# Performance work log

Hardware: AMD Instinct MI355X
Metric: run time of the kernel (lower is better)

The kernel has to match this reference:

```python
import jax, jax.numpy as jnp
import numpy as np

B, C, H, W = 8, 128, 128, 128
PLANES, K, STRIDE, PAD = 128, 3, 1, 1
BN_EPS = 1e-5


def setup_inputs() -> dict:
    key = jax.random.key(0)
    k1, k2, k3, k4 = jax.random.split(key, 4)
    x = jax.random.normal(k1, (B, C, H, W), jnp.float32)
    # ConvOffset2D: Conv2d(C, 2C, 3, pad=1, bias=False), weights ~ N(0, 0.01)
    w_off = jax.random.normal(k2, (2 * C, C, 3, 3), jnp.float32) * 0.01
    w_conv = jax.random.normal(k3, (PLANES, C, K, K), jnp.float32) * 0.05
    b_conv = jax.random.normal(k4, (PLANES,), jnp.float32) * 0.01
    gamma = jnp.ones((PLANES,), jnp.float32)
    beta = jnp.zeros((PLANES,), jnp.float32)
    return {"x": x, "w_off": w_off, "w_conv": w_conv, "b_conv": b_conv,
            "gamma": gamma, "beta": beta}


def _conv2d(x, w, stride, pad):
    return jax.lax.conv_general_dilated(
        x, w, window_strides=(stride, stride),
        padding=[(pad, pad), (pad, pad)],
        dimension_numbers=("NCHW", "OIHW", "NCHW"))


def _deform_sample(x, offsets):
    """x: (B,C,H,W); offsets: (B,2C,H,W) -> bilinear offset-sampled (B,C,H,W).
    Faithful to ConvOffset2D: raw reshape (b,2c,h,w) -> (b*c, h*w, 2),
    coords = offsets + meshgrid(i,j), clamp, bilinear interp."""
    b, c, h, w = x.shape
    off = offsets.reshape(b * c, h * w, 2)              # quirky but faithful reshape
    grid = jnp.stack(jnp.meshgrid(jnp.arange(h, dtype=x.dtype),
                                  jnp.arange(w, dtype=x.dtype),
                                  indexing="ij"), axis=-1).reshape(1, h * w, 2)
    coords = off + grid                                  # (b*c, h*w, 2)
    yc = jnp.clip(coords[..., 0], 0.0, h - 1.0)
    xc = jnp.clip(coords[..., 1], 0.0, w - 1.0)
    y0, y1 = jnp.floor(yc), jnp.ceil(yc)
    x0, x1 = jnp.floor(xc), jnp.ceil(xc)
    img = x.reshape(b * c, h * w)

    def gather(yy, xx):
        idx = (yy * w + xx).astype(jnp.int32)
        return jnp.take_along_axis(img, idx, axis=1)

    v_lt = gather(y0, x0)
    v_rb = gather(y1, x1)
    v_lb = gather(y0, x1)
    v_rt = gather(y1, x0)
    dy = yc - y0
    dx = xc - x0
    v_t = v_lt + (v_rt - v_lt) * dy   # interp along height
    v_b = v_lb + (v_rb - v_lb) * dy
    out = v_t + (v_b - v_t) * dx      # interp along width
    return out.reshape(b, c, h, w)


def reference(x, w_off, w_conv, b_conv, gamma, beta):
    offsets = _conv2d(x, w_off, 1, 1)                    # (B, 2C, H, W)
    x_off = _deform_sample(x, offsets)                   # (B, C, H, W)
    y = _conv2d(x_off, w_conv, STRIDE, PAD) + b_conv[None, :, None, None]
    y = jax.nn.relu(y)
    # BatchNorm2d in training mode: batch statistics, biased variance
    mean = y.mean(axis=(0, 2, 3), keepdims=True)
    var = jnp.square(y - mean).mean(axis=(0, 2, 3), keepdims=True)
    y = (y - mean) * jax.lax.rsqrt(var + BN_EPS)
    return y * gamma[None, :, None, None] + beta[None, :, None, None]
```

## Files before the change

### kernel.cpp

```cpp
#include <hip/hip_runtime.h>

#define B_   8
#define C_   128
#define H_   128
#define W_   128
#define HW_  16384

typedef short v8s __attribute__((ext_vector_type(8)));
typedef float v4f __attribute__((ext_vector_type(4)));

#define ROWB 4160

__device__ __forceinline__ float bf2f(unsigned short u) {
  unsigned int v = ((unsigned int)u) << 16;
  float f; __builtin_memcpy(&f, &v, 4); return f;
}
__device__ __forceinline__ unsigned short f2us(float f) {
  unsigned int u; __builtin_memcpy(&u, &f, 4);
  u += 0x7fffu + ((u >> 16) & 1u);
  return (unsigned short)(u >> 16);
}

__global__ __launch_bounds__(256) void pack_w(const float* __restrict__ w,
                                              unsigned short* __restrict__ pack,
                                              uint4* __restrict__ zb, int G) {
  if (blockIdx.x == 0) zb[threadIdx.x] = (uint4){0u, 0u, 0u, 0u};
  int idx = blockIdx.x * 256 + threadIdx.x;
  if (idx >= 20480 * G) return;
  int j  = idx & 7;
  int l  = (idx >> 3) & 63;
  int g  = (idx >> 9) % G;
  int t2 = idx / (512 * G);
  int pp = t2 % 5;
  int cc = t2 / 5;
  int oc = g * 16 + (l & 15);
  int kk = ((l >> 4) << 3) + j;
  int ic = (cc << 4) + (kk & 15);
  int rs = pp * 2 + (kk >> 4);
  float v = (rs < 9) ? w[(oc * C_ + ic) * 9 + rs] : 0.f;
  pack[idx] = f2us(v);
}

__global__ __launch_bounds__(256) void transpose_x(const float* __restrict__ x,
                                                   unsigned short* __restrict__ xt) {
  __shared__ alignas(16) unsigned short t[32 * 132];
  const int j0 = blockIdx.x * 32, i = blockIdx.y, b = blockIdx.z;
  const int tid = threadIdx.x;
  for (int e = tid; e < 128 * 32; e += 256) {
    int c = e >> 5, jj = e & 31;
    float v = x[((b * C_ + c) * H_ + i) * W_ + j0 + jj];
    t[jj * 132 + c] = f2us(v);
  }
  __syncthreads();
  for (int f = tid; f < 1024; f += 256) {
    int cg = f >> 7, g = f & 127;
    int j = g >> 2, c4 = (g & 3) << 2;
    uint2 v = *(const uint2*)&t[j * 132 + cg * 16 + c4];
    *(uint2*)(xt + ((size_t)(b * 8 + cg) * HW_ + i * W_ + j0 + j) * 16 + c4) = v;
  }
}

template <int MODE, int G>
__global__ __launch_bounds__(256) void conv_gemm(const unsigned short* __restrict__ xt,
                                                 const unsigned short* __restrict__ pack,
                                                 const float* __restrict__ bias,
                                                 const char* __restrict__ zb,
                                                 unsigned short* __restrict__ outp,
                                                 float* __restrict__ ps) {
  __shared__ alignas(16) char rawb[3 * ROWB];
  __shared__ float bs1[128], bs2[128];

  const int nb = blockIdx.x;
  int b, i, mt;
  {
    int xcd = nb & 7, r = nb >> 3;
    if (MODE == 0) { b = r >> 5; mt = (r >> 4) & 1; i = xcd * 16 + (r & 15); }
    else           { b = r >> 4; mt = 0;            i = xcd * 16 + (r & 15); }
  }
  const int tid  = threadIdx.x;
  const int lane = tid & 63, wid = tid >> 6;
  const int q = lane >> 4, n = lane & 15;
  const int wm = wid & 1, wn = wid >> 1;

  if (MODE == 1 && tid < 128) { bs1[tid] = 0.f; bs2[tid] = 0.f; }
  if (tid < 12) {
    int r = tid >> 2, rem = tid & 3, side = rem >> 1, h = rem & 1;
    *(uint4*)(rawb + r * ROWB + (side ? 129 * 32 : 0) + h * 16) = (uint4){0u,0u,0u,0u};
  }

  int boff[5];
#pragma unroll
  for (int pp = 0; pp < 5; ++pp) {
    int rs = pp * 2 + (q >> 1);
    if (rs > 8) rs = 8;
    int r = (rs >= 6) ? 2 : ((rs >= 3) ? 1 : 0);
    int s = rs - r * 3;
    boff[pp] = r * ROWB + s * 32 + (q & 1) * 16;
  }
  const int pcol = (wn * 64 + n) * 32;

  v4f acc[4][4];
#pragma unroll
  for (int a = 0; a < 4; ++a)
#pragma unroll
    for (int c = 0; c < 4; ++c) acc[a][c] = (v4f){0.f, 0.f, 0.f, 0.f};

  const v8s* packv = (const v8s*)pack;
  const int gbase = mt * 8 + wm * 4;

  v8s Acur[4];
  {
    const v8s* ap = packv + (0 * G + gbase) * 64 + lane;
#pragma unroll
    for (int fm = 0; fm < 4; ++fm) Acur[fm] = ap[fm * 64];
  }

  for (int cc = 0; cc < 8; ++cc) {
    __syncthreads();
    const char* ccbase = (const char*)xt + (size_t)(b * 8 + cc) * (HW_ * 32);
#pragma unroll
    for (int t = 0; t < 3; ++t) {
      int c = wid * 3 + t, r = c >> 2, k = c & 3;
      int ii = i + r - 1;
      const char* src = ((unsigned)ii < 128u)
                          ? ccbase + ii * 4096 + k * 1024 + lane * 16
                          : zb + lane * 16;
      __builtin_amdgcn_global_load_lds(
          (const __attribute__((address_space(1))) unsigned int*)src,
          (__attribute__((address_space(3))) unsigned int*)(rawb + r * ROWB + 32 + k * 1024),
          16, 0, 0);
    }
    __syncthreads();

#pragma unroll
    for (int pp = 0; pp < 5; ++pp) {
      v8s Anxt[4];
      const bool havenext = (pp < 4) || (cc < 7);
      if (havenext) {
        int ncc = (pp < 4) ? cc : cc + 1;
        int npp = (pp < 4) ? pp + 1 : 0;
        const v8s* ap = packv + ((ncc * 5 + npp) * G + gbase) * 64 + lane;
#pragma unroll
        for (int fm = 0; fm < 4; ++fm) Anxt[fm] = ap[fm * 64];
      }
      v8s Bf[4];
#pragma unroll
      for (int fn = 0; fn < 4; ++fn)
        Bf[fn] = *(const v8s*)(rawb + boff[pp] + pcol + fn * 512);
#pragma unroll
      for (int fm = 0; fm < 4; ++fm) {
#pragma unroll
        for (int fn = 0; fn < 4; ++fn)
          acc[fm][fn] = __builtin_amdgcn_mfma_f32_16x16x32_bf16(Acur[fm], Bf[fn],
                                                                acc[fm][fn], 0, 0, 0);
      }
      if (havenext) {
#pragma unroll
        for (int fm = 0; fm < 4; ++fm) Acur[fm] = Anxt[fm];
      }
    }
  }

  const int OC = G * 16;
  const int ob = (b * OC + mt * 128 + wm * 64) * HW_ + i * W_ + wn * 64;

  if (MODE == 0) {
#pragma unroll
    for (int fm = 0; fm < 4; ++fm)
#pragma unroll
      for (int fn = 0; fn < 4; ++fn)
#pragma unroll
        for (int rr = 0; rr < 4; ++rr)
          outp[ob + (fm * 16 + q * 4 + rr) * HW_ + fn * 16 + n] = f2us(acc[fm][fn][rr]);
  } else {
    float bv[4][4], s1a[4][4], s2a[4][4];
#pragma unroll
    for (int fm = 0; fm < 4; ++fm)
#pragma unroll
      for (int rr = 0; rr < 4; ++rr) {
        bv[fm][rr] = bias[wm * 64 + fm * 16 + q * 4 + rr];
        s1a[fm][rr] = 0.f; s2a[fm][rr] = 0.f;
      }
#pragma unroll
    for (int fm = 0; fm < 4; ++fm)
#pragma unroll
      for (int fn = 0; fn < 4; ++fn)
#pragma unroll
        for (int rr = 0; rr < 4; ++rr) {
          float v = acc[fm][fn][rr] + bv[fm][rr];
          v = fmaxf(v, 0.f);
          outp[ob + (fm * 16 + q * 4 + rr) * HW_ + fn * 16 + n] = f2us(v);
          s1a[fm][rr] += v; s2a[fm][rr] += v * v;
        }
#pragma unroll
    for (int fm = 0; fm < 4; ++fm)
#pragma unroll
      for (int rr = 0; rr < 4; ++rr) {
        float s1 = s1a[fm][rr], s2 = s2a[fm][rr];
#pragma unroll
        for (int m = 1; m < 16; m <<= 1) {
          s1 += __shfl_xor(s1, m);
          s2 += __shfl_xor(s2, m);
        }
        if (n == 0) {
          atomicAdd(&bs1[wm * 64 + fm * 16 + q * 4 + rr], s1);
          atomicAdd(&bs2[wm * 64 + fm * 16 + q * 4 + rr], s2);
        }
      }
    __syncthreads();
    if (tid < 128) {
      ps[nb * 128 + tid]          = bs1[tid];
      ps[131072 + nb * 128 + tid] = bs2[tid];
    }
  }
}

__global__ __launch_bounds__(256) void deform_t(const float* __restrict__ x,
                                                const unsigned short* __restrict__ offs,
                                                unsigned short* __restrict__ xofft) {
  __shared__ alignas(16) unsigned short t[128 * 132];
  const int i = blockIdx.x, b = blockIdx.y;
  const int tid = threadIdx.x;
  for (int e = tid; e < 16384; e += 256) {
    int c = e >> 7, j = e & 127;
    int qpix = (i << 7) + j;
    int oidx = (b << 22) + (c << 15) + 2 * qpix;
    unsigned int pr = *(const unsigned int*)(offs + oidx);
    float oy = bf2f((unsigned short)(pr & 0xffffu));
    float ox = bf2f((unsigned short)(pr >> 16));
    float yc = fminf(fmaxf(oy + (float)i, 0.f), 127.f);
    float xc = fminf(fmaxf(ox + (float)j, 0.f), 127.f);
    float y0f = floorf(yc), y1f = ceilf(yc);
    float x0f = floorf(xc), x1f = ceilf(xc);
    int y0 = (int)y0f, y1 = (int)y1f, x0 = (int)x0f, x1 = (int)x1f;
    const float* img = x + ((b * C_ + c) << 14);
    float v_lt = img[y0 * W_ + x0];
    float v_rb = img[y1 * W_ + x1];
    float v_lb = img[y0 * W_ + x1];
    float v_rt = img[y1 * W_ + x0];
    float dy = yc - y0f, dx = xc - x0f;
    float v_t = v_lt + (v_rt - v_lt) * dy;
    float v_b = v_lb + (v_rb - v_lb) * dy;
    float o   = v_t + (v_b - v_t) * dx;
    t[j * 132 + c] = f2us(o);
  }
  __syncthreads();
  for (int f = tid; f < 4096; f += 256) {
    int cg = f >> 9, g = f & 511;
    int j = g >> 2, c4 = (g & 3) << 2;
    uint2 v = *(const uint2*)&t[j * 132 + cg * 16 + c4];
    *(uint2*)(xofft + ((size_t)(b * 8 + cg) * HW_ + i * W_ + j) * 16 + c4) = v;
  }
}

__global__ __launch_bounds__(256) void bn_finalize(const float* __restrict__ ps,
                                                   const float* __restrict__ gamma,
                                                   const float* __restrict__ beta,
                                                   float* __restrict__ stats) {
  const int c = blockIdx.x, tid = threadIdx.x;
  float s1 = 0.f, s2 = 0.f;
  for (int k = tid; k < 1024; k += 256) {
    s1 += ps[k * 128 + c];
    s2 += ps[131072 + k * 128 + c];
  }
#pragma unroll
  for (int m = 32; m > 0; m >>= 1) {
    s1 += __shfl_down(s1, m);
    s2 += __shfl_down(s2, m);
  }
  __shared__ float l1[4], l2[4];
  int wid = tid >> 6;
  if ((tid & 63) == 0) { l1[wid] = s1; l2[wid] = s2; }
  __syncthreads();
  if (tid == 0) {
    s1 = l1[0] + l1[1] + l1[2] + l1[3];
    s2 = l2[0] + l2[1] + l2[2] + l2[3];
    const float invn = 1.f / 131072.f;
    float mean = s1 * invn;
    float var  = s2 * invn - mean * mean;
    float inv  = rsqrtf(var + 1e-5f);
    float sc = gamma[c] * inv;
    stats[c]       = sc;
    stats[128 + c] = beta[c] - mean * sc;
  }
}

__global__ __launch_bounds__(256) void bn_apply(const unsigned short* __restrict__ y,
                                                const float* __restrict__ stats,
                                                float* __restrict__ out) {
  int gid = blockIdx.x * 256 + threadIdx.x;
  int base = gid << 3;
  int c = (base >> 14) & 127;
  float sc = stats[c], sh = stats[128 + c];
  uint4 u = *(const uint4*)(y + base);
  const unsigned short* us = (const unsigned short*)&u;
  float4 o0, o1;
  o0.x = bf2f(us[0]) * sc + sh;  o0.y = bf2f(us[1]) * sc + sh;
  o0.z = bf2f(us[2]) * sc + sh;  o0.w = bf2f(us[3]) * sc + sh;
  o1.x = bf2f(us[4]) * sc + sh;  o1.y = bf2f(us[5]) * sc + sh;
  o1.z = bf2f(us[6]) * sc + sh;  o1.w = bf2f(us[7]) * sc + sh;
  ((float4*)out)[gid * 2]     = o0;
  ((float4*)out)[gid * 2 + 1] = o1;
}

extern "C" void kernel_launch(void* const* d_in, const int* in_sizes, int n_in,
                              void* d_out, int out_size, void* d_ws, size_t ws_size,
                              hipStream_t stream) {
  const float* x      = (const float*)d_in[0];
  const float* w_off  = (const float*)d_in[1];
  const float* w_conv = (const float*)d_in[2];
  const float* b_conv = (const float*)d_in[3];
  const float* gamma  = (const float*)d_in[4];
  const float* beta   = (const float*)d_in[5];
  float* out = (float*)d_out;

  char* ws = (char*)d_ws;
  unsigned short* x_t    = (unsigned short*)ws;
  unsigned short* xoff_t = (unsigned short*)ws;
  unsigned short* offs = (unsigned short*)(ws + 33554432);
  unsigned short* yws  = (unsigned short*)(ws + 33554432);
  float* ps    = (float*)(ws + 67108864);
  float* stats = (float*)(ws + 68157440);
  unsigned short* pack_off  = (unsigned short*)(ws + 100663296);
  unsigned short* pack_main = (unsigned short*)(ws + 101318656);
  char* zb = ws + 101646336;

  pack_w<<<80 * 16, 256, 0, stream>>>(w_off, pack_off, (uint4*)zb, 16);
  pack_w<<<80 * 8, 256, 0, stream>>>(w_conv, pack_main, (uint4*)zb, 8);
  transpose_x<<<dim3(4, 128, 8), 256, 0, stream>>>(x, x_t);
  conv_gemm<0, 16><<<2048, 256, 0, stream>>>(x_t, pack_off, nullptr, zb, offs, nullptr);
  deform_t<<<dim3(128, 8), 256, 0, stream>>>(x, offs, xoff_t);
  conv_gemm<1, 8><<<1024, 256, 0, stream>>>(xoff_t, pack_main, b_conv, zb, yws, ps);
  bn_finalize<<<128, 256, 0, stream>>>(ps, gamma, beta, stats);
  bn_apply<<<8192, 256, 0, stream>>>(yws, stats, out);
}
```

Before: 332.5 us.

## Fuse prep kernels, drop A-fragment prefetch, raise conv occupancy bound

Merges the two weight-packing launches and the input transpose into one prep kernel, which removes two kernel launches. In conv_gemm it removes the software prefetch of the next A fragments and loads them directly at each step, and it adds a launch_bounds minimum of 4 blocks per CU so the compiler limits register use. Together these aim to raise occupancy and cut launch overhead, at the cost of exposing weight-load latency that the prefetch used to hide.

```diff
diff --git a/kernel.cpp b/kernel.cpp
--- a/kernel.cpp
+++ b/kernel.cpp
@@ -21,11 +21,38 @@
   return (unsigned short)(u >> 16);
 }
 
-__global__ __launch_bounds__(256) void pack_w(const float* __restrict__ w,
-                                              unsigned short* __restrict__ pack,
-                                              uint4* __restrict__ zb, int G) {
-  if (blockIdx.x == 0) zb[threadIdx.x] = (uint4){0u, 0u, 0u, 0u};
-  int idx = blockIdx.x * 256 + threadIdx.x;
+__global__ __launch_bounds__(256) void prep(const float* __restrict__ x,
+                                            unsigned short* __restrict__ xt,
+                                            const float* __restrict__ w_off,
+                                            const float* __restrict__ w_conv,
+                                            unsigned short* __restrict__ pack_off,
+                                            unsigned short* __restrict__ pack_main,
+                                            uint4* __restrict__ zb) {
+  __shared__ alignas(16) unsigned short t[32 * 132];
+  const int bid = blockIdx.x, tid = threadIdx.x;
+  if (bid < 4096) {
+    const int j0 = (bid & 3) * 32, i = (bid >> 2) & 127, b = bid >> 9;
+    for (int e = tid; e < 128 * 32; e += 256) {
+      int c = e >> 5, jj = e & 31;
+      float v = x[((b * C_ + c) * H_ + i) * W_ + j0 + jj];
+      t[jj * 132 + c] = f2us(v);
+    }
+    __syncthreads();
+    for (int f = tid; f < 1024; f += 256) {
+      int cg = f >> 7, g = f & 127;
+      int j = g >> 2, c4 = (g & 3) << 2;
+      uint2 v = *(const uint2*)&t[j * 132 + cg * 16 + c4];
+      *(uint2*)(xt + ((size_t)(b * 8 + cg) * HW_ + i * W_ + j0 + j) * 16 + c4) = v;
+    }
+    return;
+  }
+  const int pb = bid - 4096;
+  if (pb == 0) zb[tid] = (uint4){0u, 0u, 0u, 0u};
+  const float* w;
+  unsigned short* pack;
+  int G, idx;
+  if (pb < 1280) { w = w_off;  pack = pack_off;  G = 16; idx = pb * 256 + tid; }
+  else           { w = w_conv; pack = pack_main; G = 8;  idx = (pb - 1280) * 256 + tid; }
   if (idx >= 20480 * G) return;
   int j  = idx & 7;
   int l  = (idx >> 3) & 63;
@@ -41,32 +68,13 @@
   pack[idx] = f2us(v);
 }
 
-__global__ __launch_bounds__(256) void transpose_x(const float* __restrict__ x,
-                                                   unsigned short* __restrict__ xt) {
-  __shared__ alignas(16) unsigned short t[32 * 132];
-  const int j0 = blockIdx.x * 32, i = blockIdx.y, b = blockIdx.z;
-  const int tid = threadIdx.x;
-  for (int e = tid; e < 128 * 32; e += 256) {
-    int c = e >> 5, jj = e & 31;
-    float v = x[((b * C_ + c) * H_ + i) * W_ + j0 + jj];
-    t[jj * 132 + c] = f2us(v);
-  }
-  __syncthreads();
-  for (int f = tid; f < 1024; f += 256) {
-    int cg = f >> 7, g = f & 127;
-    int j = g >> 2, c4 = (g & 3) << 2;
-    uint2 v = *(const uint2*)&t[j * 132 + cg * 16 + c4];
-    *(uint2*)(xt + ((size_t)(b * 8 + cg) * HW_ + i * W_ + j0 + j) * 16 + c4) = v;
-  }
-}
-
 template <int MODE, int G>
-__global__ __launch_bounds__(256) void conv_gemm(const unsigned short* __restrict__ xt,
-                                                 const unsigned short* __restrict__ pack,
-                                                 const float* __restrict__ bias,
-                                                 const char* __restrict__ zb,
-                                                 unsigned short* __restrict__ outp,
-                                                 float* __restrict__ ps) {
+__global__ __launch_bounds__(256, 4) void conv_gemm(const unsigned short* __restrict__ xt,
+                                                    const unsigned short* __restrict__ pack,
+                                                    const float* __restrict__ bias,
+                                                    const char* __restrict__ zb,
+                                                    unsigned short* __restrict__ outp,
+                                                    float* __restrict__ ps) {
   __shared__ alignas(16) char rawb[3 * ROWB];
   __shared__ float bs1[128], bs2[128];
 
@@ -107,13 +115,6 @@
 
   const v8s* packv = (const v8s*)pack;
   const int gbase = mt * 8 + wm * 4;
-
-  v8s Acur[4];
-  {
-    const v8s* ap = packv + (0 * G + gbase) * 64 + lane;
-#pragma unroll
-    for (int fm = 0; fm < 4; ++fm) Acur[fm] = ap[fm * 64];
-  }
 
   for (int cc = 0; cc < 8; ++cc) {
     __syncthreads();
@@ -134,15 +135,10 @@
 
 #pragma unroll
     for (int pp = 0; pp < 5; ++pp) {
-      v8s Anxt[4];
-      const bool havenext = (pp < 4) || (cc < 7);
-      if (havenext) {
-        int ncc = (pp < 4) ? cc : cc + 1;
-        int npp = (pp < 4) ? pp + 1 : 0;
-        const v8s* ap = packv + ((ncc * 5 + npp) * G + gbase) * 64 + lane;
-#pragma unroll
-        for (int fm = 0; fm < 4; ++fm) Anxt[fm] = ap[fm * 64];
-      }
+      const v8s* ap = packv + ((cc * 5 + pp) * G + gbase) * 64 + lane;
+      v8s Af[4];
+#pragma unroll
+      for (int fm = 0; fm < 4; ++fm) Af[fm] = ap[fm * 64];
       v8s Bf[4];
 #pragma unroll
       for (int fn = 0; fn < 4; ++fn)
@@ -151,12 +147,8 @@
       for (int fm = 0; fm < 4; ++fm) {
 #pragma unroll
         for (int fn = 0; fn < 4; ++fn)
-          acc[fm][fn] = __builtin_amdgcn_mfma_f32_16x16x32_bf16(Acur[fm], Bf[fn],
+          acc[fm][fn] = __builtin_amdgcn_mfma_f32_16x16x32_bf16(Af[fm], Bf[fn],
                                                                 acc[fm][fn], 0, 0, 0);
-      }
-      if (havenext) {
-#pragma unroll
-        for (int fm = 0; fm < 4; ++fm) Acur[fm] = Anxt[fm];
       }
     }
   }
@@ -325,9 +317,8 @@
   unsigned short* pack_main = (unsigned short*)(ws + 101318656);
   char* zb = ws + 101646336;
 
-  pack_w<<<80 * 16, 256, 0, stream>>>(w_off, pack_off, (uint4*)zb, 16);
-  pack_w<<<80 * 8, 256, 0, stream>>>(w_conv, pack_main, (uint4*)zb, 8);
-  transpose_x<<<dim3(4, 128, 8), 256, 0, stream>>>(x, x_t);
+  prep<<<6016, 256, 0, stream>>>(x, x_t, w_off, w_conv, pack_off, pack_main,
+                                 (uint4*)zb);
   conv_gemm<0, 16><<<2048, 256, 0, stream>>>(x_t, pack_off, nullptr, zb, offs, nullptr);
   deform_t<<<dim3(128, 8), 256, 0, stream>>>(x, offs, xoff_t);
   conv_gemm<1, 8><<<1024, 256, 0, stream>>>(xoff_t, pack_main, b_conv, zb, yws, ps);
```

Result: faster. 311.8 us (-6.2%).
